# Kernel tuning notes

Hardware: AMD Instinct MI355X
Metric: run time of the kernel (lower is better)

## Reference

```python
import jax, jax.numpy as jnp
import numpy as np

B, T, S, I, H = 64, 64, 512, 512, 512

def setup_inputs() -> dict:
    key = jax.random.key(0)
    ks = jax.random.split(key, 9)
    sc = 0.02
    return {
        "input": jax.random.normal(ks[0], (B, T, I), jnp.float32),
        "h0": jax.random.normal(ks[1], (B, H), jnp.float32),
        "c0": jax.random.normal(ks[2], (B, H), jnp.float32),
        "ctx": jax.random.normal(ks[3], (S, B, H), jnp.float32),
        "W_ih": jax.random.normal(ks[4], (4 * H, I), jnp.float32) * sc,
        "b_ih": jax.random.normal(ks[5], (4 * H,), jnp.float32) * sc,
        "W_hh": jax.random.normal(ks[6], (4 * H, H), jnp.float32) * sc,
        "b_hh": jax.random.normal(ks[7], (4 * H,), jnp.float32) * sc,
        "W_out": jax.random.normal(ks[8], (H, 2 * H), jnp.float32) * sc,
    }

def reference(input, h0, c0, ctx, W_ih, b_ih, W_hh, b_hh, W_out):
    ctx_b = ctx.transpose(1, 0, 2)          # (B, S, H)
    x_tm = input.transpose(1, 0, 2)          # (T, B, I) time-major

    def step(carry, x):
        hx, cx = carry
        gates = x @ W_ih.T + b_ih + hx @ W_hh.T + b_hh   # (B, 4H)
        i, f, g, o = jnp.split(gates, 4, axis=1)          # chunk order: in, forget, cell, out
        ct = jax.nn.sigmoid(f) * cx + jax.nn.sigmoid(i) * jnp.tanh(g)
        ht = jax.nn.sigmoid(o) * jnp.tanh(ct)
        # dot attention over source positions
        scores = jnp.einsum('bsh,bh->bs', ctx_b, ht)      # (B, S)
        attn = jax.nn.softmax(scores, axis=1)
        wc = jnp.einsum('bs,bsh->bh', attn, ctx_b)        # (B, H)
        h_tilde = jnp.tanh(jnp.concatenate([wc, ht], axis=1) @ W_out.T)
        return (ht, ct), h_tilde

    (hT, cT), out = jax.lax.scan(step, (h0, c0), x_tm)    # out: (T, B, H)
    return out.transpose(1, 0, 2), hT, cT
```

## Files before the change

### kernel.cpp

```cpp
#include <hip/hip_runtime.h>
#include <hip/hip_bf16.h>

#define NB 64
#define NT_ 64
#define NS 512
#define NI 512
#define NH 512
#define G4 2048
#define H2 1024
#define BT (NB*NT_)
#define RBLK 64
#define CPB 8
#define XWB 512
#define TRB 4096
#define WOB 128
#define ATT 128
#define GRID_MEGA (RBLK + XWB + TRB + WOB + ATT)

typedef __attribute__((ext_vector_type(8))) short short8;
typedef __attribute__((ext_vector_type(4))) float f32x4;

__device__ __forceinline__ short f2bs(float f) {
    __hip_bfloat16 h = __float2bfloat16(f);
    return *reinterpret_cast<short*>(&h);
}
__device__ __forceinline__ float bs2f(short s) {
    unsigned int u = ((unsigned int)(unsigned short)s) << 16;
    union { unsigned int u; float f; } c; c.u = u; return c.f;
}
__device__ __forceinline__ short8 ld8b(const __hip_bfloat16* p) {
    return *reinterpret_cast<const short8*>(p);
}
__device__ __forceinline__ void ld8f2(const float* p, short8& hi, short8& lo) {
    float4 a = *reinterpret_cast<const float4*>(p);
    float4 b = *reinterpret_cast<const float4*>(p + 4);
    float v[8] = {a.x,a.y,a.z,a.w,b.x,b.y,b.z,b.w};
    #pragma unroll
    for (int i = 0; i < 8; i++) {
        short h = f2bs(v[i]);
        hi[i] = h;
        lo[i] = f2bs(v[i] - bs2f(h));
    }
}
__device__ __forceinline__ float fsigm(float x){ return 1.f/(1.f + __expf(-x)); }
__device__ __forceinline__ float ftanh(float x){ float e = __expf(2.f*x); return 1.f - 2.f/(e + 1.f); }

__global__ __launch_bounds__(256) void hseq0_init(const float* __restrict__ h0,
                                                  __hip_bfloat16* __restrict__ hs_h,
                                                  __hip_bfloat16* __restrict__ hs_l,
                                                  unsigned* __restrict__ sync) {
    int i = blockIdx.x*256 + threadIdx.x;
    if (i < 4096) sync[i] = 0u;
    if (i < NB*NH) {
        float x = h0[i];
        __hip_bfloat16 h = __float2bfloat16(x);
        hs_h[i] = h;
        hs_l[i] = __float2bfloat16(x - __bfloat162float(h));
    }
}

__global__ __launch_bounds__(256, 1) void lstm_mega(
    const float* __restrict__ c0,
    const float* __restrict__ W_hh,
    const float* __restrict__ input,
    const float* __restrict__ W_ih,
    const float* __restrict__ b_ih,
    const float* __restrict__ b_hh,
    float* __restrict__ XW2,
    __hip_bfloat16* __restrict__ hs_h,
    __hip_bfloat16* __restrict__ hs_l,
    float* __restrict__ hT, float* __restrict__ cT,
    unsigned* __restrict__ flags,
    unsigned* __restrict__ xwcnt,
    unsigned* __restrict__ trcnt,
    unsigned* __restrict__ wocnt,
    const float* __restrict__ ctx,
    __hip_bfloat16* __restrict__ ctxT,
    const float* __restrict__ W_out,
    __hip_bfloat16* __restrict__ Wout_h,
    __hip_bfloat16* __restrict__ Wout_l,
    float* __restrict__ out)
{
    __shared__ __align__(16) char smem_raw[82432];
    int bid = blockIdx.x;
    int tid = threadIdx.x;
    int lane = tid & 63, w = tid >> 6;
    int fr = lane & 15, fq = lane >> 4;

    if (bid < RBLK) {
        __hip_bfloat16* Wh = (__hip_bfloat16*)smem_raw;
        __hip_bfloat16* Wl = (__hip_bfloat16*)(smem_raw + 32768);
        float (*gl)[32][33] = (float(*)[32][33])(smem_raw + 65536);
        int bi = bid;
        {
            int jl = tid >> 3, ck8 = tid & 7;
            int grow = (jl >> 3) * NH + bi * CPB + (jl & 7);
            const float* src = W_hh + (size_t)grow * NH;
            #pragma unroll
            for (int cc = 0; cc < 8; cc++) {
                int ck = ck8 * 8 + cc;
                short8 hi, lo;
                ld8f2(src + ck*8, hi, lo);
                int sw = (ck * 16) ^ ((jl & 7) << 4);
                *(short8*)((char*)Wh + jl * 1024 + sw) = hi;
                *(short8*)((char*)Wl + jl * 1024 + sw) = lo;
            }
        }
        int eb  = tid >> 2;
        int ec0 = (tid & 3) * 2;
        int ebl = eb & 31, mhalf = eb >> 5;
        float creg[2];
        creg[0] = c0[eb * NH + bi*CPB + ec0];
        creg[1] = c0[eb * NH + bi*CPB + ec0 + 1];
        {
            int guard = 0;
            while (__hip_atomic_load(&xwcnt[0], __ATOMIC_RELAXED, __HIP_MEMORY_SCOPE_AGENT) < 8u) {
                __builtin_amdgcn_s_sleep(1);
                if (++guard > (1<<22)) break;
            }
        }
        float xw[8];
        #pragma unroll
        for (int g = 0; g < 4; g++)
          #pragma unroll
          for (int u = 0; u < 2; u++)
            xw[g*2+u] = XW2[(size_t)eb*G4 + g*NH + bi*CPB + ec0 + u];
        __syncthreads();

        int m0 = (w & 1) * 32;
        int kbase = (w >> 1) * 256;

        for (int t = 0; t < NT_; t++) {
            const __hip_bfloat16* Ah = hs_h + (size_t)t * NB * NH;
            const __hip_bfloat16* Al = hs_l + (size_t)t * NB * NH;
            short8 Aregh[2][8], Aregl[2][8];
            #pragma unroll
            for (int i = 0; i < 2; i++) {
                const __hip_bfloat16* rowH = Ah + (size_t)(m0 + i*16 + fr) * NH + kbase + fq*8;
                const __hip_bfloat16* rowL = Al + (size_t)(m0 + i*16 + fr) * NH + kbase + fq*8;
                #pragma unroll
                for (int k8 = 0; k8 < 8; k8++) {
                    Aregh[i][k8] = ld8b(rowH + k8*32);
                    Aregl[i][k8] = ld8b(rowL + k8*32);
                }
            }
            f32x4 acc[2][2] = {};
            #pragma unroll
            for (int k8 = 0; k8 < 8; k8++) {
                short8 b_h[2], b_l[2];
                #pragma unroll
                for (int j = 0; j < 2; j++) {
                    int jl = j*16 + fr;
                    int byt = jl*1024 + ((((kbase + k8*32 + fq*8)*2)) ^ ((jl & 7) << 4));
                    b_h[j] = *(const short8*)((const char*)Wh + byt);
                    b_l[j] = *(const short8*)((const char*)Wl + byt);
                }
                #pragma unroll
                for (int i = 0; i < 2; i++)
                    #pragma unroll
                    for (int j = 0; j < 2; j++) {
                        acc[i][j] = __builtin_amdgcn_mfma_f32_16x16x32_bf16(Aregh[i][k8], b_h[j], acc[i][j], 0,0,0);
                        acc[i][j] = __builtin_amdgcn_mfma_f32_16x16x32_bf16(Aregh[i][k8], b_l[j], acc[i][j], 0,0,0);
                        acc[i][j] = __builtin_amdgcn_mfma_f32_16x16x32_bf16(Aregl[i][k8], b_h[j], acc[i][j], 0,0,0);
                    }
            }
            #pragma unroll
            for (int i = 0; i < 2; i++)
              #pragma unroll
              for (int j = 0; j < 2; j++)
                #pragma unroll
                for (int r = 0; r < 4; r++)
                    gl[w][i*16 + fq*4 + r][j*16 + fr] = acc[i][j][r];
            __syncthreads();

            float hv[2];
            #pragma unroll
            for (int u = 0; u < 2; u++) {
                int cl = ec0 + u;
                float gi = gl[mhalf][ebl][cl]      + gl[2+mhalf][ebl][cl]      + xw[u];
                float gf = gl[mhalf][ebl][8 + cl]  + gl[2+mhalf][ebl][8 + cl]  + xw[2+u];
                float gg = gl[mhalf][ebl][16 + cl] + gl[2+mhalf][ebl][16 + cl] + xw[4+u];
                float go = gl[mhalf][ebl][24 + cl] + gl[2+mhalf][ebl][24 + cl] + xw[6+u];
                float ct = fsigm(gf)*creg[u] + fsigm(gi)*ftanh(gg);
                hv[u] = fsigm(go)*ftanh(ct);
                creg[u] = ct;
            }
            int hcol = bi*CPB + ec0;
            size_t hoff = (size_t)(t+1)*NB*NH + (size_t)eb*NH + hcol;
            unsigned short h0b = (unsigned short)f2bs(hv[0]);
            unsigned short h1b = (unsigned short)f2bs(hv[1]);
            unsigned ph = (unsigned)h0b | ((unsigned)h1b << 16);
            unsigned short l0b = (unsigned short)f2bs(hv[0] - bs2f((short)h0b));
            unsigned short l1b = (unsigned short)f2bs(hv[1] - bs2f((short)h1b));
            unsigned pl = (unsigned)l0b | ((unsigned)l1b << 16);
            __hip_atomic_store((unsigned*)&hs_h[hoff], ph, __ATOMIC_RELAXED, __HIP_MEMORY_SCOPE_AGENT);
            __hip_atomic_store((unsigned*)&hs_l[hoff], pl, __ATOMIC_RELAXED, __HIP_MEMORY_SCOPE_AGENT);
            if (t == NT_-1) {
                *(float2*)&hT[(size_t)eb*NH + hcol] = make_float2(hv[0], hv[1]);
                *(float2*)&cT[(size_t)eb*NH + hcol] = make_float2(creg[0], creg[1]);
            }
            asm volatile("s_waitcnt vmcnt(0)" ::: "memory");
            __syncthreads();
            if (tid == 0)
                __hip_atomic_store(&flags[bi*16], (unsigned)(t+1), __ATOMIC_RELAXED, __HIP_MEMORY_SCOPE_AGENT);
            if (t + 1 < NT_) {
                int guard = 0;
                while (__hip_atomic_load(&xwcnt[(t+1)*16], __ATOMIC_RELAXED, __HIP_MEMORY_SCOPE_AGENT) < 8u) {
                    __builtin_amdgcn_s_sleep(1);
                    if (++guard > (1<<22)) break;
                }
                #pragma unroll
                for (int g = 0; g < 4; g++)
                  #pragma unroll
                  for (int u = 0; u < 2; u++)
                    xw[g*2+u] = XW2[((size_t)(t+1)*NB + eb)*G4 + g*NH + bi*CPB + ec0 + u];
            }
            {
                unsigned target = (unsigned)(t+1);
                int guard = 0;
                while (__hip_atomic_load(&flags[lane*16], __ATOMIC_RELAXED, __HIP_MEMORY_SCOPE_AGENT) < target) {
                    __builtin_amdgcn_s_sleep(1);
                    if (++guard > (1<<22)) break;
                }
            }
        }
    } else if (bid < RBLK + XWB) {
        int e  = bid - RBLK;
        int t0 = e >> 3;
        int n0 = ((e & 7) * 4 + w) * 64;
        f32x4 acc[4][4] = {};
        for (int kk = 0; kk < NI; kk += 32) {
            short8 ah[4], al[4], bh[4], bl[4];
            #pragma unroll
            for (int i = 0; i < 4; i++)
                ld8f2(input + ((size_t)(i*16+fr)*NT_ + t0)*NI + kk + fq*8, ah[i], al[i]);
            #pragma unroll
            for (int j = 0; j < 4; j++)
                ld8f2(W_ih + (size_t)(n0+j*16+fr)*NI + kk + fq*8, bh[j], bl[j]);
            #pragma unroll
            for (int i = 0; i < 4; i++)
                #pragma unroll
                for (int j = 0; j < 4; j++) {
                    acc[i][j] = __builtin_amdgcn_mfma_f32_16x16x32_bf16(ah[i], bh[j], acc[i][j], 0,0,0);
                    acc[i][j] = __builtin_amdgcn_mfma_f32_16x16x32_bf16(ah[i], bl[j], acc[i][j], 0,0,0);
                    acc[i][j] = __builtin_amdgcn_mfma_f32_16x16x32_bf16(al[i], bh[j], acc[i][j], 0,0,0);
                }
        }
        #pragma unroll
        for (int i = 0; i < 4; i++)
          #pragma unroll
          for (int j = 0; j < 4; j++)
            #pragma unroll
            for (int r = 0; r < 4; r++) {
                int b = i*16 + fq*4 + r;
                int n = n0 + j*16 + fr;
                float v = acc[i][j][r] + b_ih[n] + b_hh[n];
                union { float f; unsigned u; } cv; cv.f = v;
                __hip_atomic_store((unsigned*)&XW2[((size_t)t0*NB + b)*G4 + n], cv.u,
                                   __ATOMIC_RELAXED, __HIP_MEMORY_SCOPE_AGENT);
            }
        asm volatile("s_waitcnt vmcnt(0)" ::: "memory");
        __syncthreads();
        if (tid == 0)
            __hip_atomic_fetch_add(&xwcnt[t0*16], 1u, __ATOMIC_RELAXED, __HIP_MEMORY_SCOPE_AGENT);
    } else if (bid < RBLK + XWB + TRB) {
        float (*tile)[65] = (float(*)[65])smem_raw;
        int tr = bid - (RBLK + XWB);
        int s0 = (tr & 7) * 64, h0 = ((tr >> 3) & 7) * 64, b = tr >> 6;
        int tx = tid & 63, ty = tid >> 6;
        for (int i = 0; i < 16; i++) {
            int s = i*4 + ty;
            tile[s][tx] = ctx[(size_t)(s0+s)*NB*NH + (size_t)b*NH + h0 + tx];
        }
        __syncthreads();
        for (int i = 0; i < 8; i++) {
            int h = i*8 + (tid >> 5);
            int cp = tid & 31;
            unsigned short v0 = (unsigned short)f2bs(tile[2*cp][h]);
            unsigned short v1 = (unsigned short)f2bs(tile[2*cp+1][h]);
            unsigned pv = (unsigned)v0 | ((unsigned)v1 << 16);
            __hip_atomic_store((unsigned*)&ctxT[(size_t)b*NH*NS + (size_t)(h0+h)*NS + s0 + 2*cp],
                               pv, __ATOMIC_RELAXED, __HIP_MEMORY_SCOPE_AGENT);
        }
        asm volatile("s_waitcnt vmcnt(0)" ::: "memory");
        __syncthreads();
        if (tid == 0)
            __hip_atomic_fetch_add(&trcnt[b*16], 1u, __ATOMIC_RELAXED, __HIP_MEMORY_SCOPE_AGENT);
    } else if (bid < RBLK + XWB + TRB + WOB) {
        int wv = bid - (RBLK + XWB + TRB);
        for (int p = wv*256 + tid; p < NH*H2/2; p += WOB*256) {
            float x0 = W_out[2*p], x1 = W_out[2*p+1];
            unsigned short h0b = (unsigned short)f2bs(x0);
            unsigned short h1b = (unsigned short)f2bs(x1);
            unsigned short l0b = (unsigned short)f2bs(x0 - bs2f((short)h0b));
            unsigned short l1b = (unsigned short)f2bs(x1 - bs2f((short)h1b));
            __hip_atomic_store((unsigned*)Wout_h + p, (unsigned)h0b | ((unsigned)h1b << 16),
                               __ATOMIC_RELAXED, __HIP_MEMORY_SCOPE_AGENT);
            __hip_atomic_store((unsigned*)Wout_l + p, (unsigned)l0b | ((unsigned)l1b << 16),
                               __ATOMIC_RELAXED, __HIP_MEMORY_SCOPE_AGENT);
        }
        asm volatile("s_waitcnt vmcnt(0)" ::: "memory");
        __syncthreads();
        if (tid == 0)
            __hip_atomic_fetch_add(&wocnt[0], 1u, __ATOMIC_RELAXED, __HIP_MEMORY_SCOPE_AGENT);
    } else {
        int at = bid - (RBLK + XWB + TRB + WOB);
        int b = at >> 1;
        int halfsel = at & 1;
        float (*S)[520] = (float(*)[520])smem_raw;
        __hip_bfloat16 (*WcH)[520] = (__hip_bfloat16(*)[520])smem_raw;
        __hip_bfloat16 (*WcL)[520] = (__hip_bfloat16(*)[520])(smem_raw + 16640);
        __hip_bfloat16 (*AtH)[520] = (__hip_bfloat16(*)[520])(smem_raw + 33280);
        __hip_bfloat16 (*AtL)[520] = (__hip_bfloat16(*)[520])(smem_raw + 49920);

        {
            int guard = 0;
            while (__hip_atomic_load(&wocnt[0], __ATOMIC_RELAXED, __HIP_MEMORY_SCOPE_AGENT) < (unsigned)WOB) {
                __builtin_amdgcn_s_sleep(1);
                if (++guard > (1<<24)) break;
            }
            guard = 0;
            while (__hip_atomic_load(&trcnt[b*16], __ATOMIC_RELAXED, __HIP_MEMORY_SCOPE_AGENT) < 64u) {
                __builtin_amdgcn_s_sleep(1);
                if (++guard > (1<<24)) break;
            }
        }

        for (int tg = halfsel*2; tg < halfsel*2 + 2; tg++) {
            int t0 = tg * 16;
            {
                unsigned target = (unsigned)(t0 + 16);
                int guard = 0;
                while (__hip_atomic_load(&flags[lane*16], __ATOMIC_RELAXED, __HIP_MEMORY_SCOPE_AGENT) < target) {
                    __builtin_amdgcn_s_sleep(1);
                    if (++guard > (1<<24)) break;
                }
            }

            {
                f32x4 sacc[8] = {};
                const __hip_bfloat16* Ab = hs_h + (size_t)(t0+fr+1)*NB*NH + (size_t)b*NH;
                const __hip_bfloat16* Al2 = hs_l + (size_t)(t0+fr+1)*NB*NH + (size_t)b*NH;
                for (int kk = 0; kk < NH; kk += 32) {
                    short8 ah = ld8b(Ab + kk + fq*8);
                    short8 al = ld8b(Al2 + kk + fq*8);
                    #pragma unroll
                    for (int j = 0; j < 8; j++) {
                        short8 bh, bl;
                        ld8f2(ctx + (size_t)(w*128 + j*16 + fr)*NB*NH + (size_t)b*NH + kk + fq*8, bh, bl);
                        sacc[j] = __builtin_amdgcn_mfma_f32_16x16x32_bf16(ah, bh, sacc[j], 0,0,0);
                        sacc[j] = __builtin_amdgcn_mfma_f32_16x16x32_bf16(ah, bl, sacc[j], 0,0,0);
                        sacc[j] = __builtin_amdgcn_mfma_f32_16x16x32_bf16(al, bh, sacc[j], 0,0,0);
                    }
                }
                #pragma unroll
                for (int j = 0; j < 8; j++)
                  #pragma unroll
                  for (int r = 0; r < 4; r++)
                    S[fq*4 + r][w*128 + j*16 + fr] = sacc[j][r];
            }
            __syncthreads();

            for (int rr = 0; rr < 4; rr++) {
                int row = w*4 + rr;
                float v[8], mx = -1e30f;
                #pragma unroll
                for (int i = 0; i < 8; i++) { v[i] = S[row][lane + i*64]; mx = fmaxf(mx, v[i]); }
                #pragma unroll
                for (int off = 32; off; off >>= 1) mx = fmaxf(mx, __shfl_xor(mx, off));
                float sum = 0.f;
                #pragma unroll
                for (int i = 0; i < 8; i++) { v[i] = __expf(v[i]-mx); sum += v[i]; }
                #pragma unroll
                for (int off = 32; off; off >>= 1) sum += __shfl_xor(sum, off);
                float inv = 1.f/sum;
                #pragma unroll
                for (int i = 0; i < 8; i++) {
                    float a = v[i]*inv;
                    short hb = f2bs(a);
                    AtH[row][lane + i*64] = *(__hip_bfloat16*)&hb;
                    short lb = f2bs(a - bs2f(hb));
                    AtL[row][lane + i*64] = *(__hip_bfloat16*)&lb;
                }
            }
            __syncthreads();

            {
                f32x4 wacc[8] = {};
                const __hip_bfloat16* Bb = ctxT + (size_t)b*NH*NS;
                for (int kk = 0; kk < NS; kk += 32) {
                    short8 pah = *(const short8*)&AtH[fr][kk + fq*8];
                    short8 pal = *(const short8*)&AtL[fr][kk + fq*8];
                    #pragma unroll
                    for (int j = 0; j < 8; j++) {
                        short8 cb = ld8b(Bb + (size_t)(w*128 + j*16 + fr)*NS + kk + fq*8);
                        wacc[j] = __builtin_amdgcn_mfma_f32_16x16x32_bf16(pah, cb, wacc[j], 0,0,0);
                        wacc[j] = __builtin_amdgcn_mfma_f32_16x16x32_bf16(pal, cb, wacc[j], 0,0,0);
                    }
                }
                #pragma unroll
                for (int j = 0; j < 8; j++)
                  #pragma unroll
                  for (int r = 0; r < 4; r++) {
                    float v = wacc[j][r];
                    short hb = f2bs(v);
                    WcH[fq*4 + r][w*128 + j*16 + fr] = *(__hip_bfloat16*)&hb;
                    short lb = f2bs(v - bs2f(hb));
                    WcL[fq*4 + r][w*128 + j*16 + fr] = *(__hip_bfloat16*)&lb;
                  }
            }
            __syncthreads();

            {
                f32x4 oacc[8] = {};
                for (int kk = 0; kk < NH; kk += 32) {
                    short8 ah = *(const short8*)&WcH[fr][kk + fq*8];
                    short8 al = *(const short8*)&WcL[fr][kk + fq*8];
                    #pragma unroll
                    for (int j = 0; j < 8; j++) {
                        size_t wrow = (size_t)(w*128 + j*16 + fr)*H2 + kk + fq*8;
                        short8 bh = ld8b(Wout_h + wrow);
                        short8 bl = ld8b(Wout_l + wrow);
                        oacc[j] = __builtin_amdgcn_mfma_f32_16x16x32_bf16(ah, bh, oacc[j], 0,0,0);
                        oacc[j] = __builtin_amdgcn_mfma_f32_16x16x32_bf16(ah, bl, oacc[j], 0,0,0);
                        oacc[j] = __builtin_amdgcn_mfma_f32_16x16x32_bf16(al, bh, oacc[j], 0,0,0);
                    }
                }
                const __hip_bfloat16* A2h = hs_h + (size_t)(t0+fr+1)*NB*NH + (size_t)b*NH;
                const __hip_bfloat16* A2l = hs_l + (size_t)(t0+fr+1)*NB*NH + (size_t)b*NH;
                for (int kk = 0; kk < NH; kk += 32) {
                    short8 ah = ld8b(A2h + kk + fq*8);
                    short8 al = ld8b(A2l + kk + fq*8);
                    #pragma unroll
                    for (int j = 0; j < 8; j++) {
                        size_t wrow = (size_t)(w*128 + j*16 + fr)*H2 + NH + kk + fq*8;
                        short8 bh = ld8b(Wout_h + wrow);
                        short8 bl = ld8b(Wout_l + wrow);
                        oacc[j] = __builtin_amdgcn_mfma_f32_16x16x32_bf16(ah, bh, oacc[j], 0,0,0);
                        oacc[j] = __builtin_amdgcn_mfma_f32_16x16x32_bf16(ah, bl, oacc[j], 0,0,0);
                        oacc[j] = __builtin_amdgcn_mfma_f32_16x16x32_bf16(al, bh, oacc[j], 0,0,0);
                    }
                }
                #pragma unroll
                for (int j = 0; j < 8; j++)
                  #pragma unroll
                  for (int r = 0; r < 4; r++)
                    out[(size_t)(b*64 + t0 + fq*4 + r)*NH + w*128 + j*16 + fr] = ftanh(oacc[j][r]);
            }
            __syncthreads();
        }
    }
}


extern "C" void kernel_launch(void* const* d_in, const int* in_sizes, int n_in,
                              void* d_out, int out_size, void* d_ws, size_t ws_size,
                              hipStream_t stream) {
    const float* input = (const float*)d_in[0];
    const float* h0    = (const float*)d_in[1];
    const float* c0    = (const float*)d_in[2];
    const float* ctx   = (const float*)d_in[3];
    const float* W_ih  = (const float*)d_in[4];
    const float* b_ih  = (const float*)d_in[5];
    const float* W_hh  = (const float*)d_in[6];
    const float* b_hh  = (const float*)d_in[7];
    const float* W_out = (const float*)d_in[8];
    float* out = (float*)d_out;

    const size_t OFF_XW     = 0;
    const size_t OFF_HS_H   = 33554432;
    const size_t OFF_HS_L   = 37814272;
    const size_t OFF_SYNC   = 42074112;
    const size_t OFF_WOUT_H = 58859520;
    const size_t OFF_WOUT_L = 59908096;
    const size_t OFF_CTXT   = 60956672;
    if (ws_size < 94511104u) return;

    char* ws = (char*)d_ws;
    float*          XW2    = (float*)(ws + OFF_XW);
    __hip_bfloat16* hs_h   = (__hip_bfloat16*)(ws + OFF_HS_H);
    __hip_bfloat16* hs_l   = (__hip_bfloat16*)(ws + OFF_HS_L);
    unsigned*       sync   = (unsigned*)(ws + OFF_SYNC);
    unsigned*       flags  = sync;
    unsigned*       xwcnt  = sync + 1024;
    unsigned*       trcnt  = sync + 2048;
    unsigned*       wocnt  = sync + 3072;
    __hip_bfloat16* Wout_h = (__hip_bfloat16*)(ws + OFF_WOUT_H);
    __hip_bfloat16* Wout_l = (__hip_bfloat16*)(ws + OFF_WOUT_L);
    __hip_bfloat16* ctxT   = (__hip_bfloat16*)(ws + OFF_CTXT);

    hseq0_init<<<128, 256, 0, stream>>>(h0, hs_h, hs_l, sync);

    float* hT = out + (size_t)BT*NH;
    float* cT = hT + NB*NH;
    lstm_mega<<<GRID_MEGA, 256, 0, stream>>>(c0, W_hh, input, W_ih,
                                             b_ih, b_hh, XW2, hs_h, hs_l, hT, cT,
                                             flags, xwcnt, trcnt, wocnt,
                                             ctx, ctxT, W_out, Wout_h, Wout_l, out);
}
```

Before: 673.8 us.

## Move attention/output projection into separate kernel after recurrence

Attention, softmax, context and output projection no longer run inside the persistent mega-kernel, where they spun on flags waiting for hidden states. They now run in a separate attn_fused launch of 256 blocks, one per (batch, 16-step chunk), after the recurrence finishes. The ctx transpose and W_out split become plain stores without counters or atomics. This removes spin-wait synchronisation and gives more parallelism. In exchange, attention work no longer overlaps the serial recurrence and a second kernel launch is added.

```diff
diff --git a/kernel.cpp b/kernel.cpp
--- a/kernel.cpp
+++ b/kernel.cpp
@@ -14,8 +14,7 @@
 #define XWB 512
 #define TRB 4096
 #define WOB 128
-#define ATT 128
-#define GRID_MEGA (RBLK + XWB + TRB + WOB + ATT)
+#define GRID_MEGA (RBLK + XWB + TRB + WOB)
 
 typedef __attribute__((ext_vector_type(8))) short short8;
 typedef __attribute__((ext_vector_type(4))) float f32x4;
@@ -72,14 +71,11 @@
     float* __restrict__ hT, float* __restrict__ cT,
     unsigned* __restrict__ flags,
     unsigned* __restrict__ xwcnt,
-    unsigned* __restrict__ trcnt,
-    unsigned* __restrict__ wocnt,
     const float* __restrict__ ctx,
     __hip_bfloat16* __restrict__ ctxT,
     const float* __restrict__ W_out,
     __hip_bfloat16* __restrict__ Wout_h,
-    __hip_bfloat16* __restrict__ Wout_l,
-    float* __restrict__ out)
+    __hip_bfloat16* __restrict__ Wout_l)
 {
     __shared__ __align__(16) char smem_raw[82432];
     int bid = blockIdx.x;
@@ -273,182 +269,152 @@
             tile[s][tx] = ctx[(size_t)(s0+s)*NB*NH + (size_t)b*NH + h0 + tx];
         }
         __syncthreads();
+        for (int i = 0; i < 16; i++) {
+            int h = i*4 + ty;
+            ctxT[(size_t)b*NH*NS + (size_t)(h0+h)*NS + s0 + tx] = __float2bfloat16(tile[tx][h]);
+        }
+    } else {
+        int wv = bid - (RBLK + XWB + TRB);
+        for (int i = wv*256 + tid; i < NH*H2; i += WOB*256) {
+            float x = W_out[i];
+            __hip_bfloat16 h = __float2bfloat16(x);
+            Wout_h[i] = h;
+            Wout_l[i] = __float2bfloat16(x - __bfloat162float(h));
+        }
+    }
+}
+
+__global__ __launch_bounds__(256, 1) void attn_fused(
+    const __hip_bfloat16* __restrict__ hs_h,
+    const __hip_bfloat16* __restrict__ hs_l,
+    const float* __restrict__ ctx,
+    const __hip_bfloat16* __restrict__ ctxT,
+    const __hip_bfloat16* __restrict__ Wout_h,
+    const __hip_bfloat16* __restrict__ Wout_l,
+    float* __restrict__ out)
+{
+    __shared__ __align__(16) char smem_raw[66560];
+    float (*S)[520] = (float(*)[520])smem_raw;
+    __hip_bfloat16 (*WcH)[520] = (__hip_bfloat16(*)[520])smem_raw;
+    __hip_bfloat16 (*WcL)[520] = (__hip_bfloat16(*)[520])(smem_raw + 16640);
+    __hip_bfloat16 (*AtH)[520] = (__hip_bfloat16(*)[520])(smem_raw + 33280);
+    __hip_bfloat16 (*AtL)[520] = (__hip_bfloat16(*)[520])(smem_raw + 49920);
+
+    int b  = blockIdx.x >> 2;
+    int t0 = (blockIdx.x & 3) * 16;
+    int tid = threadIdx.x;
+    int lane = tid & 63, w = tid >> 6;
+    int fr = lane & 15, fq = lane >> 4;
+
+    {
+        f32x4 sacc[8] = {};
+        const __hip_bfloat16* Ab  = hs_h + (size_t)(t0+fr+1)*NB*NH + (size_t)b*NH;
+        const __hip_bfloat16* Al2 = hs_l + (size_t)(t0+fr+1)*NB*NH + (size_t)b*NH;
+        for (int kk = 0; kk < NH; kk += 32) {
+            short8 ah = ld8b(Ab + kk + fq*8);
+            short8 al = ld8b(Al2 + kk + fq*8);
+            #pragma unroll
+            for (int j = 0; j < 8; j++) {
+                short8 bh, bl;
+                ld8f2(ctx + (size_t)(w*128 + j*16 + fr)*NB*NH + (size_t)b*NH + kk + fq*8, bh, bl);
+                sacc[j] = __builtin_amdgcn_mfma_f32_16x16x32_bf16(ah, bh, sacc[j], 0,0,0);
+                sacc[j] = __builtin_amdgcn_mfma_f32_16x16x32_bf16(ah, bl, sacc[j], 0,0,0);
+                sacc[j] = __builtin_amdgcn_mfma_f32_16x16x32_bf16(al, bh, sacc[j], 0,0,0);
+            }
+        }
+        #pragma unroll
+        for (int j = 0; j < 8; j++)
+          #pragma unroll
+          for (int r = 0; r < 4; r++)
+            S[fq*4 + r][w*128 + j*16 + fr] = sacc[j][r];
+    }
+    __syncthreads();
+
+    for (int rr = 0; rr < 4; rr++) {
+        int row = w*4 + rr;
+        float v[8], mx = -1e30f;
+        #pragma unroll
+        for (int i = 0; i < 8; i++) { v[i] = S[row][lane + i*64]; mx = fmaxf(mx, v[i]); }
+        #pragma unroll
+        for (int off = 32; off; off >>= 1) mx = fmaxf(mx, __shfl_xor(mx, off));
+        float sum = 0.f;
+        #pragma unroll
+        for (int i = 0; i < 8; i++) { v[i] = __expf(v[i]-mx); sum += v[i]; }
+        #pragma unroll
+        for (int off = 32; off; off >>= 1) sum += __shfl_xor(sum, off);
+        float inv = 1.f/sum;
+        #pragma unroll
         for (int i = 0; i < 8; i++) {
-            int h = i*8 + (tid >> 5);
-            int cp = tid & 31;
-            unsigned short v0 = (unsigned short)f2bs(tile[2*cp][h]);
-            unsigned short v1 = (unsigned short)f2bs(tile[2*cp+1][h]);
-            unsigned pv = (unsigned)v0 | ((unsigned)v1 << 16);
-            __hip_atomic_store((unsigned*)&ctxT[(size_t)b*NH*NS + (size_t)(h0+h)*NS + s0 + 2*cp],
-                               pv, __ATOMIC_RELAXED, __HIP_MEMORY_SCOPE_AGENT);
-        }
-        asm volatile("s_waitcnt vmcnt(0)" ::: "memory");
-        __syncthreads();
-        if (tid == 0)
-            __hip_atomic_fetch_add(&trcnt[b*16], 1u, __ATOMIC_RELAXED, __HIP_MEMORY_SCOPE_AGENT);
-    } else if (bid < RBLK + XWB + TRB + WOB) {
-        int wv = bid - (RBLK + XWB + TRB);
-        for (int p = wv*256 + tid; p < NH*H2/2; p += WOB*256) {
-            float x0 = W_out[2*p], x1 = W_out[2*p+1];
-            unsigned short h0b = (unsigned short)f2bs(x0);
-            unsigned short h1b = (unsigned short)f2bs(x1);
-            unsigned short l0b = (unsigned short)f2bs(x0 - bs2f((short)h0b));
-            unsigned short l1b = (unsigned short)f2bs(x1 - bs2f((short)h1b));
-            __hip_atomic_store((unsigned*)Wout_h + p, (unsigned)h0b | ((unsigned)h1b << 16),
-                               __ATOMIC_RELAXED, __HIP_MEMORY_SCOPE_AGENT);
-            __hip_atomic_store((unsigned*)Wout_l + p, (unsigned)l0b | ((unsigned)l1b << 16),
-                               __ATOMIC_RELAXED, __HIP_MEMORY_SCOPE_AGENT);
-        }
-        asm volatile("s_waitcnt vmcnt(0)" ::: "memory");
-        __syncthreads();
-        if (tid == 0)
-            __hip_atomic_fetch_add(&wocnt[0], 1u, __ATOMIC_RELAXED, __HIP_MEMORY_SCOPE_AGENT);
-    } else {
-        int at = bid - (RBLK + XWB + TRB + WOB);
-        int b = at >> 1;
-        int halfsel = at & 1;
-        float (*S)[520] = (float(*)[520])smem_raw;
-        __hip_bfloat16 (*WcH)[520] = (__hip_bfloat16(*)[520])smem_raw;
-        __hip_bfloat16 (*WcL)[520] = (__hip_bfloat16(*)[520])(smem_raw + 16640);
-        __hip_bfloat16 (*AtH)[520] = (__hip_bfloat16(*)[520])(smem_raw + 33280);
-        __hip_bfloat16 (*AtL)[520] = (__hip_bfloat16(*)[520])(smem_raw + 49920);
-
-        {
-            int guard = 0;
-            while (__hip_atomic_load(&wocnt[0], __ATOMIC_RELAXED, __HIP_MEMORY_SCOPE_AGENT) < (unsigned)WOB) {
-                __builtin_amdgcn_s_sleep(1);
-                if (++guard > (1<<24)) break;
-            }
-            guard = 0;
-            while (__hip_atomic_load(&trcnt[b*16], __ATOMIC_RELAXED, __HIP_MEMORY_SCOPE_AGENT) < 64u) {
-                __builtin_amdgcn_s_sleep(1);
-                if (++guard > (1<<24)) break;
-            }
-        }
-
-        for (int tg = halfsel*2; tg < halfsel*2 + 2; tg++) {
-            int t0 = tg * 16;
-            {
-                unsigned target = (unsigned)(t0 + 16);
-                int guard = 0;
-                while (__hip_atomic_load(&flags[lane*16], __ATOMIC_RELAXED, __HIP_MEMORY_SCOPE_AGENT) < target) {
-                    __builtin_amdgcn_s_sleep(1);
-                    if (++guard > (1<<24)) break;
-                }
-            }
-
-            {
-                f32x4 sacc[8] = {};
-                const __hip_bfloat16* Ab = hs_h + (size_t)(t0+fr+1)*NB*NH + (size_t)b*NH;
-                const __hip_bfloat16* Al2 = hs_l + (size_t)(t0+fr+1)*NB*NH + (size_t)b*NH;
-                for (int kk = 0; kk < NH; kk += 32) {
-                    short8 ah = ld8b(Ab + kk + fq*8);
-                    short8 al = ld8b(Al2 + kk + fq*8);
-                    #pragma unroll
-                    for (int j = 0; j < 8; j++) {
-                        short8 bh, bl;
-                        ld8f2(ctx + (size_t)(w*128 + j*16 + fr)*NB*NH + (size_t)b*NH + kk + fq*8, bh, bl);
-                        sacc[j] = __builtin_amdgcn_mfma_f32_16x16x32_bf16(ah, bh, sacc[j], 0,0,0);
-                        sacc[j] = __builtin_amdgcn_mfma_f32_16x16x32_bf16(ah, bl, sacc[j], 0,0,0);
-                        sacc[j] = __builtin_amdgcn_mfma_f32_16x16x32_bf16(al, bh, sacc[j], 0,0,0);
-                    }
-                }
-                #pragma unroll
-                for (int j = 0; j < 8; j++)
-                  #pragma unroll
-                  for (int r = 0; r < 4; r++)
-                    S[fq*4 + r][w*128 + j*16 + fr] = sacc[j][r];
-            }
-            __syncthreads();
-
-            for (int rr = 0; rr < 4; rr++) {
-                int row = w*4 + rr;
-                float v[8], mx = -1e30f;
-                #pragma unroll
-                for (int i = 0; i < 8; i++) { v[i] = S[row][lane + i*64]; mx = fmaxf(mx, v[i]); }
-                #pragma unroll
-                for (int off = 32; off; off >>= 1) mx = fmaxf(mx, __shfl_xor(mx, off));
-                float sum = 0.f;
-                #pragma unroll
-                for (int i = 0; i < 8; i++) { v[i] = __expf(v[i]-mx); sum += v[i]; }
-                #pragma unroll
-                for (int off = 32; off; off >>= 1) sum += __shfl_xor(sum, off);
-                float inv = 1.f/sum;
-                #pragma unroll
-                for (int i = 0; i < 8; i++) {
-                    float a = v[i]*inv;
-                    short hb = f2bs(a);
-                    AtH[row][lane + i*64] = *(__hip_bfloat16*)&hb;
-                    short lb = f2bs(a - bs2f(hb));
-                    AtL[row][lane + i*64] = *(__hip_bfloat16*)&lb;
-                }
-            }
-            __syncthreads();
-
-            {
-                f32x4 wacc[8] = {};
-                const __hip_bfloat16* Bb = ctxT + (size_t)b*NH*NS;
-                for (int kk = 0; kk < NS; kk += 32) {
-                    short8 pah = *(const short8*)&AtH[fr][kk + fq*8];
-                    short8 pal = *(const short8*)&AtL[fr][kk + fq*8];
-                    #pragma unroll
-                    for (int j = 0; j < 8; j++) {
-                        short8 cb = ld8b(Bb + (size_t)(w*128 + j*16 + fr)*NS + kk + fq*8);
-                        wacc[j] = __builtin_amdgcn_mfma_f32_16x16x32_bf16(pah, cb, wacc[j], 0,0,0);
-                        wacc[j] = __builtin_amdgcn_mfma_f32_16x16x32_bf16(pal, cb, wacc[j], 0,0,0);
-                    }
-                }
-                #pragma unroll
-                for (int j = 0; j < 8; j++)
-                  #pragma unroll
-                  for (int r = 0; r < 4; r++) {
-                    float v = wacc[j][r];
-                    short hb = f2bs(v);
-                    WcH[fq*4 + r][w*128 + j*16 + fr] = *(__hip_bfloat16*)&hb;
-                    short lb = f2bs(v - bs2f(hb));
-                    WcL[fq*4 + r][w*128 + j*16 + fr] = *(__hip_bfloat16*)&lb;
-                  }
-            }
-            __syncthreads();
-
-            {
-                f32x4 oacc[8] = {};
-                for (int kk = 0; kk < NH; kk += 32) {
-                    short8 ah = *(const short8*)&WcH[fr][kk + fq*8];
-                    short8 al = *(const short8*)&WcL[fr][kk + fq*8];
-                    #pragma unroll
-                    for (int j = 0; j < 8; j++) {
-                        size_t wrow = (size_t)(w*128 + j*16 + fr)*H2 + kk + fq*8;
-                        short8 bh = ld8b(Wout_h + wrow);
-                        short8 bl = ld8b(Wout_l + wrow);
-                        oacc[j] = __builtin_amdgcn_mfma_f32_16x16x32_bf16(ah, bh, oacc[j], 0,0,0);
-                        oacc[j] = __builtin_amdgcn_mfma_f32_16x16x32_bf16(ah, bl, oacc[j], 0,0,0);
-                        oacc[j] = __builtin_amdgcn_mfma_f32_16x16x32_bf16(al, bh, oacc[j], 0,0,0);
-                    }
-                }
-                const __hip_bfloat16* A2h = hs_h + (size_t)(t0+fr+1)*NB*NH + (size_t)b*NH;
-                const __hip_bfloat16* A2l = hs_l + (size_t)(t0+fr+1)*NB*NH + (size_t)b*NH;
-                for (int kk = 0; kk < NH; kk += 32) {
-                    short8 ah = ld8b(A2h + kk + fq*8);
-                    short8 al = ld8b(A2l + kk + fq*8);
-                    #pragma unroll
-                    for (int j = 0; j < 8; j++) {
-                        size_t wrow = (size_t)(w*128 + j*16 + fr)*H2 + NH + kk + fq*8;
-                        short8 bh = ld8b(Wout_h + wrow);
-                        short8 bl = ld8b(Wout_l + wrow);
-                        oacc[j] = __builtin_amdgcn_mfma_f32_16x16x32_bf16(ah, bh, oacc[j], 0,0,0);
-                        oacc[j] = __builtin_amdgcn_mfma_f32_16x16x32_bf16(ah, bl, oacc[j], 0,0,0);
-                        oacc[j] = __builtin_amdgcn_mfma_f32_16x16x32_bf16(al, bh, oacc[j], 0,0,0);
-                    }
-                }
-                #pragma unroll
-                for (int j = 0; j < 8; j++)
-                  #pragma unroll
-                  for (int r = 0; r < 4; r++)
-                    out[(size_t)(b*64 + t0 + fq*4 + r)*NH + w*128 + j*16 + fr] = ftanh(oacc[j][r]);
-            }
-            __syncthreads();
-        }
+            float a = v[i]*inv;
+            short hb = f2bs(a);
+            AtH[row][lane + i*64] = *(__hip_bfloat16*)&hb;
+            short lb = f2bs(a - bs2f(hb));
+            AtL[row][lane + i*64] = *(__hip_bfloat16*)&lb;
+        }
+    }
+    __syncthreads();
+
+    {
+        f32x4 wacc[8] = {};
+        const __hip_bfloat16* Bb = ctxT + (size_t)b*NH*NS;
+        for (int kk = 0; kk < NS; kk += 32) {
+            short8 pah = *(const short8*)&AtH[fr][kk + fq*8];
+            short8 pal = *(const short8*)&AtL[fr][kk + fq*8];
+            #pragma unroll
+            for (int j = 0; j < 8; j++) {
+                short8 cb = ld8b(Bb + (size_t)(w*128 + j*16 + fr)*NS + kk + fq*8);
+                wacc[j] = __builtin_amdgcn_mfma_f32_16x16x32_bf16(pah, cb, wacc[j], 0,0,0);
+                wacc[j] = __builtin_amdgcn_mfma_f32_16x16x32_bf16(pal, cb, wacc[j], 0,0,0);
+            }
+        }
+        #pragma unroll
+        for (int j = 0; j < 8; j++)
+          #pragma unroll
+          for (int r = 0; r < 4; r++) {
+            float v = wacc[j][r];
+            short hb = f2bs(v);
+            WcH[fq*4 + r][w*128 + j*16 + fr] = *(__hip_bfloat16*)&hb;
+            short lb = f2bs(v - bs2f(hb));
+            WcL[fq*4 + r][w*128 + j*16 + fr] = *(__hip_bfloat16*)&lb;
+          }
+    }
+    __syncthreads();
+
+    {
+        f32x4 oacc[8] = {};
+        for (int kk = 0; kk < NH; kk += 32) {
+            short8 ah = *(const short8*)&WcH[fr][kk + fq*8];
+            short8 al = *(const short8*)&WcL[fr][kk + fq*8];
+            #pragma unroll
+            for (int j = 0; j < 8; j++) {
+                size_t wrow = (size_t)(w*128 + j*16 + fr)*H2 + kk + fq*8;
+                short8 bh = ld8b(Wout_h + wrow);
+                short8 bl = ld8b(Wout_l + wrow);
+                oacc[j] = __builtin_amdgcn_mfma_f32_16x16x32_bf16(ah, bh, oacc[j], 0,0,0);
+                oacc[j] = __builtin_amdgcn_mfma_f32_16x16x32_bf16(ah, bl, oacc[j], 0,0,0);
+                oacc[j] = __builtin_amdgcn_mfma_f32_16x16x32_bf16(al, bh, oacc[j], 0,0,0);
+            }
+        }
+        const __hip_bfloat16* A2h = hs_h + (size_t)(t0+fr+1)*NB*NH + (size_t)b*NH;
+        const __hip_bfloat16* A2l = hs_l + (size_t)(t0+fr+1)*NB*NH + (size_t)b*NH;
+        for (int kk = 0; kk < NH; kk += 32) {
+            short8 ah = ld8b(A2h + kk + fq*8);
+            short8 al = ld8b(A2l + kk + fq*8);
+            #pragma unroll
+            for (int j = 0; j < 8; j++) {
+                size_t wrow = (size_t)(w*128 + j*16 + fr)*H2 + NH + kk + fq*8;
+                short8 bh = ld8b(Wout_h + wrow);
+                short8 bl = ld8b(Wout_l + wrow);
+                oacc[j] = __builtin_amdgcn_mfma_f32_16x16x32_bf16(ah, bh, oacc[j], 0,0,0);
+                oacc[j] = __builtin_amdgcn_mfma_f32_16x16x32_bf16(ah, bl, oacc[j], 0,0,0);
+                oacc[j] = __builtin_amdgcn_mfma_f32_16x16x32_bf16(al, bh, oacc[j], 0,0,0);
+            }
+        }
+        #pragma unroll
+        for (int j = 0; j < 8; j++)
+          #pragma unroll
+          for (int r = 0; r < 4; r++)
+            out[(size_t)(b*64 + t0 + fq*4 + r)*NH + w*128 + j*16 + fr] = ftanh(oacc[j][r]);
     }
 }
 
@@ -483,8 +449,6 @@
     unsigned*       sync   = (unsigned*)(ws + OFF_SYNC);
     unsigned*       flags  = sync;
     unsigned*       xwcnt  = sync + 1024;
-    unsigned*       trcnt  = sync + 2048;
-    unsigned*       wocnt  = sync + 3072;
     __hip_bfloat16* Wout_h = (__hip_bfloat16*)(ws + OFF_WOUT_H);
     __hip_bfloat16* Wout_l = (__hip_bfloat16*)(ws + OFF_WOUT_L);
     __hip_bfloat16* ctxT   = (__hip_bfloat16*)(ws + OFF_CTXT);
@@ -495,6 +459,7 @@
     float* cT = hT + NB*NH;
     lstm_mega<<<GRID_MEGA, 256, 0, stream>>>(c0, W_hh, input, W_ih,
                                              b_ih, b_hh, XW2, hs_h, hs_l, hT, cT,
-                                             flags, xwcnt, trcnt, wocnt,
-                                             ctx, ctxT, W_out, Wout_h, Wout_l, out);
-}
+                                             flags, xwcnt, ctx, ctxT, W_out, Wout_h, Wout_l);
+
+    attn_fused<<<256, 256, 0, stream>>>(hs_h, hs_l, ctx, ctxT, Wout_h, Wout_l, out);
+}
```

Measured after the change: 614.9 us. 1.1x faster.
